# Kernel tuning notes

Measured on AMD Instinct MI355X. Metric: run time of the kernel, lower is better.

Reference implementation:

```python
import jax, jax.numpy as jnp
import numpy as np


def _topk_corr(h_s, h_t, k):
    """DGMC top-k correspondence: similarity matmul -> top-k -> gather -> dot -> softmax.

    h_s: [B, Ns, C], h_t: [B, Nt, C].
    Mirrors __top_k__ (S_ij = x_s @ x_t^T; topk indices) followed by the
    torch.gather of top-k target embeddings and S_hat = (h_s * h_t[idx]).sum(-1).
    """
    S = jnp.einsum('bsc,btc->bst', h_s, h_t)            # [B, Ns, Nt]
    _, idx = jax.lax.top_k(S, k)                         # [B, Ns, k] (largest sims)
    gathered = jax.vmap(lambda ht, ix: ht[ix])(h_t, idx)  # [B, Ns, k, C]
    S_hat = jnp.einsum('bsc,bskc->bsk', h_s, gathered)    # [B, Ns, k]
    S0 = jax.nn.softmax(S_hat, axis=-1)                   # softmax over k candidates
    return S0, idx


def setup_inputs() -> dict:
    key = jax.random.key(0)
    ks = jax.random.split(key, 4)
    B, Ns, Nt, C = 1, 10000, 10000, 256
    return {
        'eh_s': jax.random.normal(ks[0], (B, Ns, C), jnp.float32),
        'eh_t': jax.random.normal(ks[1], (B, Nt, C), jnp.float32),
        'rh_s': jax.random.normal(ks[2], (B, Ns, C), jnp.float32),
        'rh_t': jax.random.normal(ks[3], (B, Nt, C), jnp.float32),
        'k': 10,
    }


def reference(eh_s, eh_t, rh_s, rh_t, k):
    eS0, eidx = _topk_corr(eh_s, eh_t, k)
    rS0, ridx = _topk_corr(rh_s, rh_t, k)
    # to_sparse via the (all-true, single-graph) dense-batch mask: [B,Ns,k] -> [B*Ns,k]
    B, Ns, kk = eS0.shape
    return eS0.reshape(B * Ns, kk), rS0.reshape(B * Ns, kk), eidx, ridx
```

## Files before the change

kernel.cpp:

```cpp
#include <hip/hip_runtime.h>


typedef __attribute__((ext_vector_type(8)))  short bf16x8;
typedef __attribute__((ext_vector_type(16))) float f32x16;
typedef __attribute__((ext_vector_type(8)))  unsigned short u16x8;

#define K_TOP 10
#define CAND_M 12
#define CDIM 256

#define GLD_LDS(src, dst) \
    __builtin_amdgcn_global_load_lds((const __attribute__((address_space(1))) void*)(src), \
                                     (__attribute__((address_space(3))) void*)(dst), 16, 0, 0)

__device__ __forceinline__ unsigned short f2bf(float f) {
    unsigned u = __float_as_uint(f);
    u += 0x7fffu + ((u >> 16) & 1u);
    return (unsigned short)(u >> 16);
}

__device__ __forceinline__ unsigned umax2(unsigned a, unsigned b) { return a > b ? a : b; }
__device__ __forceinline__ unsigned umax3(unsigned a, unsigned b, unsigned c) {
    return umax2(umax2(a, b), c);
}

__device__ __forceinline__ unsigned umax16(const unsigned (&p)[16]) {
    unsigned x0 = umax3(p[0],  p[1],  p[2]);
    unsigned x1 = umax3(p[3],  p[4],  p[5]);
    unsigned x2 = umax3(p[6],  p[7],  p[8]);
    unsigned x3 = umax3(p[9],  p[10], p[11]);
    unsigned x4 = umax3(p[12], p[13], p[14]);
    return umax2(umax3(x0, x1, x2), umax3(x3, x4, p[15]));
}

template <int K>
__device__ __forceinline__ void sorted_insert(unsigned (&tv)[K], unsigned v) {
    bool m[K];
#pragma unroll
    for (int q = 0; q < K; ++q) m[q] = tv[q] >= v;
    unsigned nv[K];
    nv[0] = m[0] ? tv[0] : v;
#pragma unroll
    for (int q = 1; q < K; ++q)
        nv[q] = m[q] ? tv[q] : (m[q - 1] ? v : tv[q - 1]);
#pragma unroll
    for (int q = 0; q < K; ++q) tv[q] = nv[q];
}

__device__ __forceinline__ void sorted_insert2(unsigned (&tk)[CAND_M], int (&tt)[CAND_M],
                                               unsigned k, int t) {
    bool m[CAND_M];
#pragma unroll
    for (int q = 0; q < CAND_M; ++q) m[q] = tk[q] >= k;
    unsigned nk[CAND_M]; int nt[CAND_M];
    nk[0] = m[0] ? tk[0] : k;
    nt[0] = m[0] ? tt[0] : t;
#pragma unroll
    for (int q = 1; q < CAND_M; ++q) {
        nk[q] = m[q] ? tk[q] : (m[q - 1] ? k : tk[q - 1]);
        nt[q] = m[q] ? tt[q] : (m[q - 1] ? t : tt[q - 1]);
    }
#pragma unroll
    for (int q = 0; q < CAND_M; ++q) { tk[q] = nk[q]; tt[q] = nt[q]; }
}

__global__ void conv_swz(const float* __restrict__ in, unsigned short* __restrict__ out, int N)
{
    int gid = blockIdx.x * blockDim.x + threadIdx.x;
    int row = gid >> 5, gl = gid & 31;
    if (row >= N) return;
    const float4* src = (const float4*)(in + (size_t)row * CDIM + gl * 8);
    float4 a0 = src[0], a1 = src[1];
    u16x8 o;
    o[0] = f2bf(a0.x); o[1] = f2bf(a0.y); o[2] = f2bf(a0.z); o[3] = f2bf(a0.w);
    o[4] = f2bf(a1.x); o[5] = f2bf(a1.y); o[6] = f2bf(a1.z); o[7] = f2bf(a1.w);
    *(u16x8*)(out + (size_t)row * CDIM + ((gl ^ (row & 31)) * 8)) = o;
}

__device__ __forceinline__ void stage32(const unsigned short* __restrict__ htb,
                                        short* ldsbuf, int tbase, int Nt,
                                        int tid, int wbase) {
#pragma unroll
    for (int it = 0; it < 4; ++it) {
        int pp = it * 256 + tid;
        int rr = pp >> 5, gg = pp & 31;
        int grow = tbase + rr; grow = grow < Nt ? grow : Nt - 1;
        GLD_LDS(htb + (size_t)grow * CDIM + gg * 8, ldsbuf + (it * 256 + wbase) * 8);
    }
}

__global__ __launch_bounds__(256, 3) void topk_mfma(
    const float* __restrict__ ehs, const float* __restrict__ rhs_,
    const unsigned short* __restrict__ ehtb, const unsigned short* __restrict__ rhtb,
    unsigned* __restrict__ partials, int Ns, int Nt, int Pt, int SB, int PS,
    unsigned VMASK)
{
    __shared__ short ldsT[2 * 32 * 256];

    const int tid = threadIdx.x;
    const int w = tid >> 6, lane = tid & 63;
    const int l5 = lane & 31, hi = lane >> 5;
    const int wbase = tid & ~63;
    const int CH = 2 * Pt;

    const int bid  = blockIdx.x;
    const int prob = bid / (Pt * SB);
    const int rem  = bid % (Pt * SB);
    const int p    = rem / SB, sb = rem % SB;

    const float* hs = prob ? rhs_ : ehs;
    const unsigned short* htb = prob ? rhtb : ehtb;

    const int srow = sb * 128 + w * 32 + l5;
    const int srd  = srow < Ns ? srow : Ns - 1;

    bf16x8 b[16];
#pragma unroll
    for (int kk = 0; kk < 16; ++kk) {
        const float4* sp = (const float4*)(hs + (size_t)srd * CDIM + kk * 16 + hi * 8);
        float4 f0 = sp[0], f1 = sp[1];
        bf16x8 t;
        t[0] = (short)f2bf(f0.x); t[1] = (short)f2bf(f0.y);
        t[2] = (short)f2bf(f0.z); t[3] = (short)f2bf(f0.w);
        t[4] = (short)f2bf(f1.x); t[5] = (short)f2bf(f1.y);
        t[6] = (short)f2bf(f1.z); t[7] = (short)f2bf(f1.w);
        b[kk] = t;
    }

    const int t0 = p * PS;
    const int t1 = min(t0 + PS, Nt);

    unsigned tvp[K_TOP];
#pragma unroll
    for (int q = 0; q < K_TOP; ++q) tvp[q] = 0u;

    const int rounds = (t1 > t0) ? ((t1 - t0 + 31) >> 5) : 0;

    if (rounds > 0) {
        stage32(htb, ldsT, t0, Nt, tid, wbase);
        __syncthreads();

        for (int rd = 0; rd < rounds; ++rd) {
            const int cur = rd & 1;
            const int tb  = t0 + rd * 32;
            if (rd + 1 < rounds)
                stage32(htb, ldsT + (cur ^ 1) * 8192, tb + 32, Nt, tid, wbase);

            const bool guard = (tb + 32 > t1);
            const short* rowp = ldsT + cur * 8192 + l5 * CDIM;
            f32x16 acc;
#pragma unroll
            for (int r = 0; r < 16; ++r) acc[r] = 256.0f;
#pragma unroll
            for (int kk = 0; kk < 16; ++kk) {
                bf16x8 a = *(const bf16x8*)(rowp + (((kk * 2 + hi) ^ l5) * 8));
                acc = __builtin_amdgcn_mfma_f32_32x32x16_bf16(a, b[kk], acc, 0, 0, 0);
            }
            const unsigned ibase = (unsigned)(rd << 4);
            unsigned pu[16];
#pragma unroll
            for (int r = 0; r < 16; ++r)
                pu[r] = (__float_as_uint(acc[r]) & VMASK) | (ibase + (unsigned)r);
            if (guard) {
#pragma unroll
                for (int r = 0; r < 16; ++r) {
                    int t = tb + 4 * hi + (r & 3) + 8 * (r >> 2);
                    if (t >= t1) pu[r] = 0u;
                }
            }
            unsigned mx = umax16(pu);
            while (__any((int)(mx > tvp[K_TOP - 1]))) {
                sorted_insert<K_TOP>(tvp, mx);
#pragma unroll
                for (int r = 0; r < 16; ++r)
                    pu[r] = (pu[r] == mx) ? 0u : pu[r];
                mx = umax16(pu);
            }
            __syncthreads();
        }
    }

    if (srow < Ns) {
        unsigned* wp = partials + ((size_t)(prob * CH + (p * 2 + hi)) * K_TOP) * Ns + srow;
#pragma unroll
        for (int q = 0; q < K_TOP; ++q) wp[(size_t)q * Ns] = tvp[q];
    }
}

__global__ void topk_mergecand(const unsigned* __restrict__ partials, int* __restrict__ cand,
                               int Ns, int CH, int PS, unsigned rdMask)
{
    int g = blockIdx.x * blockDim.x + threadIdx.x;
    if (g >= 2 * Ns) return;
    const int prob = g >= Ns ? 1 : 0;
    const int row  = g - prob * Ns;
    const unsigned* src = partials + ((size_t)prob * CH * K_TOP) * Ns + row;

    unsigned tvk[CAND_M]; int tvt[CAND_M];
#pragma unroll
    for (int q = 0; q < CAND_M; ++q) { tvk[q] = 0u; tvt[q] = 0; }

    for (int c = 0; c < CH; ++c) {
        const int tbase = (c >> 1) * PS + 4 * (c & 1);
#pragma unroll
        for (int q = 0; q < K_TOP; ++q) {
            unsigned k = src[(size_t)(c * K_TOP + q) * Ns];
            if (k > tvk[CAND_M - 1]) {
                unsigned rd = (k >> 4) & rdMask;
                unsigned r  = k & 15u;
                int t = tbase + (int)rd * 32 + (int)((r & 3) + 8 * (r >> 2));
                sorted_insert2(tvk, tvt, k, t);
            }
        }
    }
    int* dst = cand + (size_t)g * CAND_M;
#pragma unroll
    for (int q = 0; q < CAND_M; ++q) dst[q] = tvt[q];
}

__global__ __launch_bounds__(256) void topk_refine(
    const float* __restrict__ ehs, const float* __restrict__ eht,
    const float* __restrict__ rhs_, const float* __restrict__ rht,
    const int* __restrict__ cand, float* __restrict__ out, int Ns)
{
    __shared__ double svd[CAND_M];
    __shared__ int    sci[CAND_M];

    const int wid = blockIdx.x;
    const int tid = threadIdx.x;
    const int m = tid >> 4, c = tid & 15;

    const int prob = wid < Ns ? 0 : 1;
    const int row  = prob ? (wid - Ns) : wid;
    const float* hs = prob ? rhs_ : ehs;
    const float* ht = prob ? rht  : eht;

    if (m < CAND_M) {
        const int t = cand[(size_t)wid * CAND_M + m];
        const float4* ap = (const float4*)(hs + (size_t)row * CDIM);
        const float4* bp = (const float4*)(ht + (size_t)t   * CDIM);

        double s = 0.0;
#pragma unroll
        for (int i = 0; i < 4; ++i) {
            float4 av = ap[c + 16 * i];
            float4 bv = bp[c + 16 * i];
            s += (double)av.x * (double)bv.x + (double)av.y * (double)bv.y
               + (double)av.z * (double)bv.z + (double)av.w * (double)bv.w;
        }
        s += __shfl_xor(s, 1, 64);
        s += __shfl_xor(s, 2, 64);
        s += __shfl_xor(s, 4, 64);
        s += __shfl_xor(s, 8, 64);
        if (c == 0) { svd[m] = s; sci[m] = t; }
    }
    __syncthreads();

    if (tid < 16) {
        const bool act = tid < CAND_M;
        const double sm = act ? svd[tid] : -1.0e300;
        const int    tm = act ? sci[tid] : 0x7FFFFFFF;
        int rank = 0; double vmax = -1.0e300;
#pragma unroll
        for (int j = 0; j < CAND_M; ++j) {
            double vj = svd[j]; int cj = sci[j];
            bool better = (vj > sm) || (vj == sm && cj < tm);
            rank += better ? 1 : 0;
            vmax = fmax(vmax, vj);
        }
        float ex = (act && rank < K_TOP) ? __expf((float)(sm - vmax)) : 0.f;
        float ssum = ex;
        ssum += __shfl_xor(ssum, 1, 64);
        ssum += __shfl_xor(ssum, 2, 64);
        ssum += __shfl_xor(ssum, 4, 64);
        ssum += __shfl_xor(ssum, 8, 64);
        if (act && rank < K_TOP) {
            size_t nsk = (size_t)Ns * K_TOP;
            size_t so  = (size_t)wid * K_TOP;
            out[so + rank] = ex / ssum;
            out[2 * nsk + so + rank] = (float)tm;
        }
    }
}

extern "C" void kernel_launch(void* const* d_in, const int* in_sizes, int n_in,
                              void* d_out, int out_size, void* d_ws, size_t ws_size,
                              hipStream_t stream) {
    (void)n_in; (void)out_size;
    const float* eh_s = (const float*)d_in[0];
    const float* eh_t = (const float*)d_in[1];
    const float* rh_s = (const float*)d_in[2];
    const float* rh_t = (const float*)d_in[3];

    const int Ns = in_sizes[0] / CDIM;
    const int Nt = in_sizes[1] / CDIM;
    const int SB = (Ns + 127) / 128;

    const size_t htbElems = (size_t)Nt * CDIM;
    const size_t htbBytes = 2 * htbElems * 2;
    const size_t candBytes = (size_t)2 * Ns * CAND_M * sizeof(int);

    int Pt = 14;
    while (Pt > 1 &&
           htbBytes + (size_t)2 * Ns * (2 * Pt) * K_TOP * sizeof(unsigned) + candBytes > ws_size)
        Pt -= 1;
    const int PS = (int)((((size_t)Nt + Pt - 1) / Pt + 31) & ~(size_t)31);

    int rdbits = 0;
    while ((1 << rdbits) < (PS >> 5)) ++rdbits;
    const int IDXB = 4 + rdbits;
    const unsigned VMASK  = ~((1u << IDXB) - 1u);
    const unsigned rdMask = (1u << rdbits) - 1u;

    unsigned short* htb_e = (unsigned short*)d_ws;
    unsigned short* htb_r = htb_e + htbElems;
    unsigned* partials = (unsigned*)(htb_r + htbElems);
    int*  cand = (int*)((char*)partials + (size_t)2 * Ns * (2 * Pt) * K_TOP * sizeof(unsigned));

    dim3 block(256);

    int convBlocks = (Nt * 32 + 255) / 256;
    conv_swz<<<dim3(convBlocks), block, 0, stream>>>(eh_t, htb_e, Nt);
    conv_swz<<<dim3(convBlocks), block, 0, stream>>>(rh_t, htb_r, Nt);

    topk_mfma<<<dim3(2 * Pt * SB), block, 0, stream>>>(eh_s, rh_s, htb_e, htb_r,
                                                       partials, Ns, Nt, Pt, SB, PS,
                                                       VMASK);

    int nrows = 2 * Ns;
    topk_mergecand<<<dim3((nrows + 255) / 256), block, 0, stream>>>(partials, cand,
                                                                    Ns, 2 * Pt, PS, rdMask);

    topk_refine<<<dim3(nrows), block, 0, stream>>>(eh_s, eh_t, rh_s, rh_t,
                                                   cand, (float*)d_out, Ns);
}
```

Measured before the change: 331.8 us.

## Software-pipeline MFMA compute with top-k extraction of previous round

Double-buffers the MFMA accumulator so round N's similarity tile is computed while round N-1's scores are packed and inserted into the running top-k. This is meant to hide MFMA latency behind the scalar selection work. The tail-guard masking is applied only to the final round after the loop. It costs an extra 16-float accumulator in registers, which may pressure occupancy under the launch bounds.

```diff
diff --git a/kernel.cpp b/kernel.cpp
--- a/kernel.cpp
+++ b/kernel.cpp
@@ -8,6 +8,7 @@
 #define K_TOP 10
 #define CAND_M 12
 #define CDIM 256
+#define LDS_HALF 8192
 
 #define GLD_LDS(src, dst) \
     __builtin_amdgcn_global_load_lds((const __attribute__((address_space(1))) void*)(src), \
@@ -95,7 +96,7 @@
     unsigned* __restrict__ partials, int Ns, int Nt, int Pt, int SB, int PS,
     unsigned VMASK)
 {
-    __shared__ short ldsT[2 * 32 * 256];
+    __shared__ short ldsT[2 * LDS_HALF];
 
     const int tid = threadIdx.x;
     const int w = tid >> 6, lane = tid & 63;
@@ -139,29 +140,69 @@
     if (rounds > 0) {
         stage32(htb, ldsT, t0, Nt, tid, wbase);
         __syncthreads();
-
-        for (int rd = 0; rd < rounds; ++rd) {
-            const int cur = rd & 1;
-            const int tb  = t0 + rd * 32;
-            if (rd + 1 < rounds)
-                stage32(htb, ldsT + (cur ^ 1) * 8192, tb + 32, Nt, tid, wbase);
-
-            const bool guard = (tb + 32 > t1);
-            const short* rowp = ldsT + cur * 8192 + l5 * CDIM;
-            f32x16 acc;
-#pragma unroll
-            for (int r = 0; r < 16; ++r) acc[r] = 256.0f;
+        if (rounds > 1)
+            stage32(htb, ldsT + LDS_HALF, t0 + 32, Nt, tid, wbase);
+
+        f32x16 accA, accB;
+        {
+            const short* rowp = ldsT + l5 * CDIM;
+#pragma unroll
+            for (int r = 0; r < 16; ++r) accA[r] = 256.0f;
 #pragma unroll
             for (int kk = 0; kk < 16; ++kk) {
                 bf16x8 a = *(const bf16x8*)(rowp + (((kk * 2 + hi) ^ l5) * 8));
-                acc = __builtin_amdgcn_mfma_f32_32x32x16_bf16(a, b[kk], acc, 0, 0, 0);
-            }
-            const unsigned ibase = (unsigned)(rd << 4);
+                accA = __builtin_amdgcn_mfma_f32_32x32x16_bf16(a, b[kk], accA, 0, 0, 0);
+            }
+        }
+        __syncthreads();
+
+#define BODY(OLD, NEW, RD) {                                                      \
+            if ((RD) + 1 < rounds)                                                \
+                stage32(htb, ldsT + (((RD) + 1) & 1) * LDS_HALF,                  \
+                        t0 + ((RD) + 1) * 32, Nt, tid, wbase);                    \
+            const short* rowp_ = ldsT + ((RD) & 1) * LDS_HALF + l5 * CDIM;        \
+            const unsigned ibase_ = (unsigned)(((RD) - 1) << 4);                  \
+            unsigned pu[16];                                                      \
+            _Pragma("unroll")                                                     \
+            for (int r = 0; r < 16; ++r) NEW[r] = 256.0f;                         \
+            _Pragma("unroll")                                                     \
+            for (int kk = 0; kk < 16; ++kk) {                                     \
+                bf16x8 a = *(const bf16x8*)(rowp_ + (((kk * 2 + hi) ^ l5) * 8));  \
+                NEW = __builtin_amdgcn_mfma_f32_32x32x16_bf16(a, b[kk], NEW,      \
+                                                              0, 0, 0);           \
+                pu[kk] = (__float_as_uint(OLD[kk]) & VMASK)                       \
+                         | (ibase_ + (unsigned)kk);                               \
+            }                                                                     \
+            unsigned mx = umax16(pu);                                             \
+            while (__any((int)(mx > tvp[K_TOP - 1]))) {                           \
+                sorted_insert<K_TOP>(tvp, mx);                                    \
+                _Pragma("unroll")                                                 \
+                for (int r = 0; r < 16; ++r) pu[r] = (pu[r] == mx) ? 0u : pu[r];  \
+                mx = umax16(pu);                                                  \
+            }                                                                     \
+            __syncthreads();                                                      \
+        }
+
+        int rd = 1;
+        for (; rd + 1 < rounds; rd += 2) {
+            BODY(accA, accB, rd);
+            BODY(accB, accA, (rd + 1));
+        }
+        bool lastInB = false;
+        if (rd < rounds) { BODY(accA, accB, rd); lastInB = true; }
+#undef BODY
+
+        {
+            const int rdl = rounds - 1;
+            const int tb  = t0 + rdl * 32;
+            const unsigned ibase = (unsigned)(rdl << 4);
             unsigned pu[16];
 #pragma unroll
-            for (int r = 0; r < 16; ++r)
-                pu[r] = (__float_as_uint(acc[r]) & VMASK) | (ibase + (unsigned)r);
-            if (guard) {
+            for (int r = 0; r < 16; ++r) {
+                float v = lastInB ? accB[r] : accA[r];
+                pu[r] = (__float_as_uint(v) & VMASK) | (ibase + (unsigned)r);
+            }
+            if (tb + 32 > t1) {
 #pragma unroll
                 for (int r = 0; r < 16; ++r) {
                     int t = tb + 4 * hi + (r & 3) + 8 * (r >> 2);
@@ -176,7 +217,6 @@
                     pu[r] = (pu[r] == mx) ? 0u : pu[r];
                 mx = umax16(pu);
             }
-            __syncthreads();
         }
     }
 
```

Measured after the change: 558.6 us. +68.4%, slower.
